# Kernel tuning notes

Hardware: AMD Instinct MI355X
Metric: run time of the kernel (lower is better)

Reference implementation:

```python
import jax, jax.numpy as jnp
import numpy as np

NUM_HEADS = 16


def setup_inputs() -> dict:
    key = jax.random.key(0)
    k1, k2, k3 = jax.random.split(key, 3)
    B, N, C = 2, 2048, 1024
    x = jax.random.normal(k1, (B, N, C), dtype=jnp.float32)
    w_qkv = jax.random.normal(k2, (3 * C, C), dtype=jnp.float32) * (C ** -0.5)
    w_proj = jax.random.normal(k3, (C, C), dtype=jnp.float32) * (C ** -0.5)
    b_proj = jnp.zeros((C,), dtype=jnp.float32)
    return {"x": x, "w_qkv": w_qkv, "w_proj": w_proj, "b_proj": b_proj}


def reference(x, w_qkv, w_proj, b_proj):
    B, N, C = x.shape
    H = NUM_HEADS
    D = C // H
    scale = 1.0 / jnp.sqrt(jnp.asarray(D, x.dtype))
    qkv = (x @ w_qkv.T).reshape(B, N, 3, H, D)
    qkv = jnp.transpose(qkv, (2, 0, 3, 1, 4))  # [3,B,H,N,D]
    q, k, v = qkv[0], qkv[1], qkv[2]
    # scaled dot-product attention with explicit score matrix [B,H,N,N]
    attn = jnp.einsum('bhnd,bhmd->bhnm', q, k) * scale
    attn = jax.nn.softmax(attn, axis=-1)
    out = jnp.einsum('bhnm,bhmd->bhnd', attn, v)
    out = jnp.transpose(out, (0, 2, 1, 3)).reshape(B, N, C)
    # output projection
    return out @ w_proj.T + b_proj
```

## Files before the change

### kernel.cpp

```cpp
#include <hip/hip_runtime.h>

typedef unsigned short u16;
typedef __attribute__((ext_vector_type(8))) short bf16x8;
typedef __attribute__((ext_vector_type(4))) float f32x4;

#define B_ 2
#define N_ 2048
#define C_ 1024
#define H_ 16
#define D_ 64
#define M_ (B_ * N_)

#define QSCALE 0.18033688011114336f

#define EXP2R(x) __builtin_amdgcn_exp2f(x)

__device__ __forceinline__ u16 f2bf(float f) {
    union { float f; unsigned u; } x; x.f = f;
    return (u16)((x.u + 0x8000u) >> 16);
}
__device__ __forceinline__ unsigned pack2bf(float a, float b) {
    union { float f; unsigned u; } x, y; x.f = a; y.f = b;
    return __builtin_amdgcn_perm(y.u + 0x8000u, x.u + 0x8000u, 0x07060302);
}

__device__ __forceinline__ void async_copy16(const void* gsrc, void* ldst) {
    __builtin_amdgcn_global_load_lds(
        (__attribute__((address_space(1))) void*)gsrc,
        (__attribute__((address_space(3))) void*)ldst,
        16, 0, 0);
}

__global__ void cast3_kernel(const float* __restrict__ x, const float* __restrict__ wq,
                             const float* __restrict__ wp, u16* __restrict__ xo,
                             u16* __restrict__ wqo, u16* __restrict__ wpo) {
    int b = blockIdx.x;
    const float* s; u16* d;
    if (b < 4096)      { s = x;  d = xo;  }
    else if (b < 7168) { s = wq; d = wqo; b -= 4096; }
    else               { s = wp; d = wpo; b -= 7168; }
    int i = (b * 256 + threadIdx.x) * 4;
    const float4 v = *(const float4*)(s + i);
    uint2 o;
    o.x = pack2bf(v.x, v.y);
    o.y = pack2bf(v.z, v.w);
    *(uint2*)(d + i) = o;
}

template <int EPI>
__global__ __launch_bounds__(256, 2) void gemm_bt(
    const u16* __restrict__ A, const u16* __restrict__ Bm,
    int M, int Ncols, int K, int ntiles_n,
    u16* __restrict__ qo, u16* __restrict__ ko, u16* __restrict__ vt,
    const float* __restrict__ bias, float* __restrict__ out) {
    __shared__ u16 As[128 * 64];
    __shared__ u16 Bs[128 * 64];
    const int tid = threadIdx.x, lane = tid & 63, w = tid >> 6;
    const int bx = blockIdx.x % ntiles_n, by = blockIdx.x / ntiles_n;
    const int m0 = by * 128, n0 = bx * 128;
    const int wm = w >> 1, wn = w & 1;
    const int q16 = lane >> 4, l15 = lane & 15;
    const int r0 = lane >> 3, c0 = (lane & 7) * 8;
    f32x4 acc[4][4] = {};

    for (int k0 = 0; k0 < K; k0 += 64) {
#pragma unroll
        for (int i = 0; i < 4; ++i) {
            int blk = w * 4 + i;
            int r = blk * 8 + r0;
            async_copy16(A + (size_t)(m0 + r) * K + k0 + c0, (char*)As + blk * 1024);
            async_copy16(Bm + (size_t)(n0 + r) * K + k0 + c0, (char*)Bs + blk * 1024);
        }
        __builtin_amdgcn_s_waitcnt(0);
        __syncthreads();
#pragma unroll
        for (int ks = 0; ks < 2; ++ks) {
            bf16x8 af[4], bf[4];
#pragma unroll
            for (int i = 0; i < 4; ++i) {
                af[i] = *(const bf16x8*)&As[(wm * 64 + i * 16 + l15) * 64 + ks * 32 + q16 * 8];
                bf[i] = *(const bf16x8*)&Bs[(wn * 64 + i * 16 + l15) * 64 + ks * 32 + q16 * 8];
            }
#pragma unroll
            for (int mi = 0; mi < 4; ++mi)
#pragma unroll
                for (int ni = 0; ni < 4; ++ni)
                    acc[mi][ni] = __builtin_amdgcn_mfma_f32_16x16x32_bf16(af[mi], bf[ni], acc[mi][ni], 0, 0, 0);
        }
        __syncthreads();
    }

#pragma unroll
    for (int mi = 0; mi < 4; ++mi) {
#pragma unroll
        for (int ni = 0; ni < 4; ++ni) {
            int n_g = n0 + wn * 64 + ni * 16 + l15;
            if (EPI == 0) {
                int which = n_g >> 10;
                int h = (n_g >> 6) & 15;
                int d = n_g & 63;
                int m_base = m0 + wm * 64 + mi * 16 + q16 * 4;
                int b = m_base >> 11;
                int nn0 = m_base & 2047;
                if (which == 2) {
                    uint2 pk;
                    pk.x = pack2bf(acc[mi][ni][0], acc[mi][ni][1]);
                    pk.y = pack2bf(acc[mi][ni][2], acc[mi][ni][3]);
                    *(uint2*)(vt + ((size_t)((b * H_ + h) * D_ + d) << 11) + nn0) = pk;
                } else {
                    size_t base = ((size_t)((b * H_ + h) * N_ + nn0) << 6) + d;
#pragma unroll
                    for (int r = 0; r < 4; ++r) {
                        float v = acc[mi][ni][r];
                        if (which == 0) qo[base + (size_t)r * D_] = f2bf(v * QSCALE);
                        else            ko[base + (size_t)r * D_] = f2bf(v);
                    }
                }
            } else {
#pragma unroll
                for (int r = 0; r < 4; ++r) {
                    int m_g = m0 + wm * 64 + mi * 16 + q16 * 4 + r;
                    out[(size_t)m_g * Ncols + n_g] = acc[mi][ni][r] + bias[n_g];
                }
            }
        }
    }
}

__global__ __launch_bounds__(256, 3) void attn_kernel(
    const u16* __restrict__ Q, const u16* __restrict__ K,
    const u16* __restrict__ VT, u16* __restrict__ O) {
    __shared__ u16 Ks[2][64 * 64];
    __shared__ u16 Vs[2][64 * 64];
    __shared__ u16 Ps[4][32 * 68];
    const int tid = threadIdx.x, lane = tid & 63, w = tid >> 6;
    const int q16 = lane >> 4, l15 = lane & 15;
    const int l7 = l15 & 7;
    const int bh = blockIdx.x >> 4;
    const int q0 = (blockIdx.x & 15) * 128;
    const size_t head = (size_t)bh * N_ * D_;
    const int lr3 = lane >> 3, lc7 = lane & 7;

    auto stage = [&](int kt, int buf) {
        int key0 = kt * 64;
#pragma unroll
        for (int i = 0; i < 2; ++i) {
            int c = w * 2 + i;
            int row = c * 8 + lr3;
            async_copy16(K + head + (size_t)(key0 + row) * D_ + (lc7 ^ lr3) * 8,
                         (char*)Ks[buf] + c * 1024);
            async_copy16(VT + head + (size_t)row * N_ + key0 + (lc7 ^ lr3) * 8,
                         (char*)Vs[buf] + c * 1024);
        }
    };

    stage(0, 0);
    bf16x8 qf[2][2];
#pragma unroll
    for (int f = 0; f < 2; ++f)
#pragma unroll
        for (int ks = 0; ks < 2; ++ks)
            qf[f][ks] = *(const bf16x8*)(Q + head + (size_t)(q0 + w * 32 + f * 16 + l15) * D_ +
                                         ks * 32 + q16 * 8);
    __builtin_amdgcn_s_waitcnt(0);
    __syncthreads();

    f32x4 o_acc[2][4] = {};
    float rs[2] = {0.f, 0.f};

    for (int kt = 0; kt < 32; ++kt) {
        int buf = kt & 1;
        if (kt + 1 < 32) stage(kt + 1, buf ^ 1);

#pragma unroll
        for (int kb = 0; kb < 4; ++kb) {
            f32x4 st[2] = {};
#pragma unroll
            for (int ks = 0; ks < 2; ++ks) {
                bf16x8 kf = *(const bf16x8*)&Ks[buf][(kb * 16 + l15) * 64 + ((ks * 4 + q16) ^ l7) * 8];
#pragma unroll
                for (int f = 0; f < 2; ++f)
                    st[f] = __builtin_amdgcn_mfma_f32_16x16x32_bf16(kf, qf[f][ks], st[f], 0, 0, 0);
            }
#pragma unroll
            for (int f = 0; f < 2; ++f) {
                float p0 = EXP2R(st[f][0]), p1 = EXP2R(st[f][1]);
                float p2 = EXP2R(st[f][2]), p3 = EXP2R(st[f][3]);
                rs[f] += (p0 + p1) + (p2 + p3);
                uint2 pk;
                pk.x = pack2bf(p0, p1);
                pk.y = pack2bf(p2, p3);
                *(uint2*)&Ps[w][(f * 16 + l15) * 68 + kb * 16 + q16 * 4] = pk;
            }
        }
#pragma unroll
        for (int ks2 = 0; ks2 < 2; ++ks2) {
            bf16x8 pf[2];
#pragma unroll
            for (int f = 0; f < 2; ++f)
                pf[f] = *(const bf16x8*)&Ps[w][(f * 16 + l15) * 68 + ks2 * 32 + q16 * 8];
#pragma unroll
            for (int di = 0; di < 4; ++di) {
                bf16x8 vf = *(const bf16x8*)&Vs[buf][(di * 16 + l15) * 64 + ((ks2 * 4 + q16) ^ l7) * 8];
#pragma unroll
                for (int f = 0; f < 2; ++f)
                    o_acc[f][di] = __builtin_amdgcn_mfma_f32_16x16x32_bf16(pf[f], vf, o_acc[f][di], 0, 0, 0);
            }
        }
        __builtin_amdgcn_s_waitcnt(0);
        __syncthreads();
    }

#pragma unroll
    for (int f = 0; f < 2; ++f) {
        rs[f] += __shfl_xor(rs[f], 16);
        rs[f] += __shfl_xor(rs[f], 32);
    }

    const int b = bh >> 4, h = bh & 15;
#pragma unroll
    for (int f = 0; f < 2; ++f) {
        float inv[4];
#pragma unroll
        for (int r = 0; r < 4; ++r) inv[r] = 1.0f / __shfl(rs[f], q16 * 4 + r);
#pragma unroll
        for (int di = 0; di < 4; ++di) {
            int d = di * 16 + l15;
#pragma unroll
            for (int r = 0; r < 4; ++r) {
                int qg = q0 + w * 32 + f * 16 + q16 * 4 + r;
                O[((size_t)(b * N_ + qg) << 10) + h * 64 + d] = f2bf(o_acc[f][di][r] * inv[r]);
            }
        }
    }
}

extern "C" void kernel_launch(void* const* d_in, const int* in_sizes, int n_in,
                              void* d_out, int out_size, void* d_ws, size_t ws_size,
                              hipStream_t stream) {
    const float* x      = (const float*)d_in[0];
    const float* w_qkv  = (const float*)d_in[1];
    const float* w_proj = (const float*)d_in[2];
    const float* b_proj = (const float*)d_in[3];
    float* out = (float*)d_out;

    char* ws = (char*)d_ws;
    const size_t MB = 1024 * 1024;
    u16* x_bf     = (u16*)(ws + 0 * MB);
    u16* wqkv_bf  = (u16*)(ws + 8 * MB);
    u16* wproj_bf = (u16*)(ws + 14 * MB);
    u16* q_bf     = (u16*)(ws + 16 * MB);
    u16* k_bf     = (u16*)(ws + 24 * MB);
    u16* vt_bf    = (u16*)(ws + 32 * MB);
    u16* ao_bf    = (u16*)(ws + 40 * MB);

    cast3_kernel<<<8192, 256, 0, stream>>>(x, w_qkv, w_proj, x_bf, wqkv_bf, wproj_bf);

    gemm_bt<0><<<32 * 24, 256, 0, stream>>>(x_bf, wqkv_bf, M_, 3 * C_, C_, 24,
                                            q_bf, k_bf, vt_bf, nullptr, nullptr);

    attn_kernel<<<512, 256, 0, stream>>>(q_bf, k_bf, vt_bf, ao_bf);

    gemm_bt<1><<<32 * 8, 256, 0, stream>>>(ao_bf, wproj_bf, M_, C_, C_, 8,
                                           nullptr, nullptr, nullptr, b_proj, out);
}
```

Baseline: 200.5 us.

## Split attention key range across two wave groups with LDS merge of partials

The attention block grows to 512 threads. Two groups of four waves each process half of the key sequence for the same 128 queries, and their unnormalized outputs and row sums are combined through shared memory at the end. The double-buffered async prefetch is replaced by single-buffer load-then-compute per group, which exposes load latency that more resident waves must hide. The GEMM launch bound is raised to 3 blocks per CU to push occupancy, which may cost registers.

```diff
diff --git a/kernel.cpp b/kernel.cpp
--- a/kernel.cpp
+++ b/kernel.cpp
@@ -48,7 +48,7 @@
 }
 
 template <int EPI>
-__global__ __launch_bounds__(256, 2) void gemm_bt(
+__global__ __launch_bounds__(256, 3) void gemm_bt(
     const u16* __restrict__ A, const u16* __restrict__ Bm,
     int M, int Ncols, int K, int ntiles_n,
     u16* __restrict__ qo, u16* __restrict__ ko, u16* __restrict__ vt,
@@ -127,57 +127,58 @@
     }
 }
 
-__global__ __launch_bounds__(256, 3) void attn_kernel(
+__global__ __launch_bounds__(512, 4) void attn_kernel(
     const u16* __restrict__ Q, const u16* __restrict__ K,
     const u16* __restrict__ VT, u16* __restrict__ O) {
-    __shared__ u16 Ks[2][64 * 64];
-    __shared__ u16 Vs[2][64 * 64];
-    __shared__ u16 Ps[4][32 * 68];
+    __shared__ __align__(16) char smem[67584];
+    u16* Ks = (u16*)smem;
+    u16* Vs = (u16*)(smem + 16384);
+    u16* Ps = (u16*)(smem + 32768);
+    float* Cn = (float*)smem;
+    float* Cl = (float*)(smem + 33792);
     const int tid = threadIdx.x, lane = tid & 63, w = tid >> 6;
+    const int g = w >> 2, wq = w & 3;
     const int q16 = lane >> 4, l15 = lane & 15;
     const int l7 = l15 & 7;
     const int bh = blockIdx.x >> 4;
     const int q0 = (blockIdx.x & 15) * 128;
     const size_t head = (size_t)bh * N_ * D_;
     const int lr3 = lane >> 3, lc7 = lane & 7;
-
-    auto stage = [&](int kt, int buf) {
-        int key0 = kt * 64;
+    u16* Ksg = Ks + g * 4096;
+    u16* Vsg = Vs + g * 4096;
+    u16* Psw = Ps + w * (32 * 68);
+
+    bf16x8 qf[2][2];
+#pragma unroll
+    for (int f = 0; f < 2; ++f)
+#pragma unroll
+        for (int ks = 0; ks < 2; ++ks)
+            qf[f][ks] = *(const bf16x8*)(Q + head + (size_t)(q0 + wq * 32 + f * 16 + l15) * D_ +
+                                         ks * 32 + q16 * 8);
+
+    f32x4 o_acc[2][4] = {};
+    float rs[2] = {0.f, 0.f};
+
+    for (int ktl = 0; ktl < 16; ++ktl) {
+        int key0 = g * 1024 + ktl * 64;
 #pragma unroll
         for (int i = 0; i < 2; ++i) {
-            int c = w * 2 + i;
+            int c = wq * 2 + i;
             int row = c * 8 + lr3;
             async_copy16(K + head + (size_t)(key0 + row) * D_ + (lc7 ^ lr3) * 8,
-                         (char*)Ks[buf] + c * 1024);
+                         (char*)Ksg + c * 1024);
             async_copy16(VT + head + (size_t)row * N_ + key0 + (lc7 ^ lr3) * 8,
-                         (char*)Vs[buf] + c * 1024);
-        }
-    };
-
-    stage(0, 0);
-    bf16x8 qf[2][2];
-#pragma unroll
-    for (int f = 0; f < 2; ++f)
-#pragma unroll
-        for (int ks = 0; ks < 2; ++ks)
-            qf[f][ks] = *(const bf16x8*)(Q + head + (size_t)(q0 + w * 32 + f * 16 + l15) * D_ +
-                                         ks * 32 + q16 * 8);
-    __builtin_amdgcn_s_waitcnt(0);
-    __syncthreads();
-
-    f32x4 o_acc[2][4] = {};
-    float rs[2] = {0.f, 0.f};
-
-    for (int kt = 0; kt < 32; ++kt) {
-        int buf = kt & 1;
-        if (kt + 1 < 32) stage(kt + 1, buf ^ 1);
+                         (char*)Vsg + c * 1024);
+        }
+        __builtin_amdgcn_s_waitcnt(0);
+        __syncthreads();
 
 #pragma unroll
         for (int kb = 0; kb < 4; ++kb) {
             f32x4 st[2] = {};
 #pragma unroll
             for (int ks = 0; ks < 2; ++ks) {
-                bf16x8 kf = *(const bf16x8*)&Ks[buf][(kb * 16 + l15) * 64 + ((ks * 4 + q16) ^ l7) * 8];
+                bf16x8 kf = *(const bf16x8*)&Ksg[(kb * 16 + l15) * 64 + ((ks * 4 + q16) ^ l7) * 8];
 #pragma unroll
                 for (int f = 0; f < 2; ++f)
                     st[f] = __builtin_amdgcn_mfma_f32_16x16x32_bf16(kf, qf[f][ks], st[f], 0, 0, 0);
@@ -190,7 +191,7 @@
                 uint2 pk;
                 pk.x = pack2bf(p0, p1);
                 pk.y = pack2bf(p2, p3);
-                *(uint2*)&Ps[w][(f * 16 + l15) * 68 + kb * 16 + q16 * 4] = pk;
+                *(uint2*)&Psw[(f * 16 + l15) * 68 + kb * 16 + q16 * 4] = pk;
             }
         }
 #pragma unroll
@@ -198,16 +199,15 @@
             bf16x8 pf[2];
 #pragma unroll
             for (int f = 0; f < 2; ++f)
-                pf[f] = *(const bf16x8*)&Ps[w][(f * 16 + l15) * 68 + ks2 * 32 + q16 * 8];
+                pf[f] = *(const bf16x8*)&Psw[(f * 16 + l15) * 68 + ks2 * 32 + q16 * 8];
 #pragma unroll
             for (int di = 0; di < 4; ++di) {
-                bf16x8 vf = *(const bf16x8*)&Vs[buf][(di * 16 + l15) * 64 + ((ks2 * 4 + q16) ^ l7) * 8];
+                bf16x8 vf = *(const bf16x8*)&Vsg[(di * 16 + l15) * 64 + ((ks2 * 4 + q16) ^ l7) * 8];
 #pragma unroll
                 for (int f = 0; f < 2; ++f)
                     o_acc[f][di] = __builtin_amdgcn_mfma_f32_16x16x32_bf16(pf[f], vf, o_acc[f][di], 0, 0, 0);
             }
         }
-        __builtin_amdgcn_s_waitcnt(0);
         __syncthreads();
     }
 
@@ -217,19 +217,39 @@
         rs[f] += __shfl_xor(rs[f], 32);
     }
 
-    const int b = bh >> 4, h = bh & 15;
-#pragma unroll
-    for (int f = 0; f < 2; ++f) {
-        float inv[4];
-#pragma unroll
-        for (int r = 0; r < 4; ++r) inv[r] = 1.0f / __shfl(rs[f], q16 * 4 + r);
-#pragma unroll
-        for (int di = 0; di < 4; ++di) {
-            int d = di * 16 + l15;
-#pragma unroll
-            for (int r = 0; r < 4; ++r) {
-                int qg = q0 + w * 32 + f * 16 + q16 * 4 + r;
-                O[((size_t)(b * N_ + qg) << 10) + h * 64 + d] = f2bf(o_acc[f][di][r] * inv[r]);
+    if (g == 1) {
+#pragma unroll
+        for (int f = 0; f < 2; ++f) {
+#pragma unroll
+            for (int di = 0; di < 4; ++di)
+#pragma unroll
+                for (int r = 0; r < 4; ++r)
+                    Cn[(wq * 32 + f * 16 + q16 * 4 + r) * 66 + di * 16 + l15] = o_acc[f][di][r];
+        }
+        if (q16 == 0) {
+            Cl[wq * 32 + l15] = rs[0];
+            Cl[wq * 32 + 16 + l15] = rs[1];
+        }
+    }
+    __syncthreads();
+    if (g == 0) {
+        const int b = bh >> 4, h = bh & 15;
+#pragma unroll
+        for (int f = 0; f < 2; ++f) {
+            float inv[4];
+#pragma unroll
+            for (int r = 0; r < 4; ++r)
+                inv[r] = 1.0f / (__shfl(rs[f], q16 * 4 + r) + Cl[wq * 32 + f * 16 + q16 * 4 + r]);
+#pragma unroll
+            for (int di = 0; di < 4; ++di) {
+                int d = di * 16 + l15;
+#pragma unroll
+                for (int r = 0; r < 4; ++r) {
+                    int qg = q0 + wq * 32 + f * 16 + q16 * 4 + r;
+                    float num = o_acc[f][di][r] +
+                                Cn[(wq * 32 + f * 16 + q16 * 4 + r) * 66 + d];
+                    O[((size_t)(b * N_ + qg) << 10) + h * 64 + d] = f2bf(num * inv[r]);
+                }
             }
         }
     }
@@ -259,7 +279,7 @@
     gemm_bt<0><<<32 * 24, 256, 0, stream>>>(x_bf, wqkv_bf, M_, 3 * C_, C_, 24,
                                             q_bf, k_bf, vt_bf, nullptr, nullptr);
 
-    attn_kernel<<<512, 256, 0, stream>>>(q_bf, k_bf, vt_bf, ao_bf);
+    attn_kernel<<<512, 512, 0, stream>>>(q_bf, k_bf, vt_bf, ao_bf);
 
     gemm_bt<1><<<32 * 8, 256, 0, stream>>>(ao_bf, wproj_bf, M_, C_, C_, 8,
                                            nullptr, nullptr, nullptr, b_proj, out);
```

Result: slower. 206.7 us (+3.1%).

## Halve attention query tile to 64 rows and double grid, swizzle P buffer

Applied to the files above, without the earlier changes.

The attention kernel now gives each wave 16 query rows instead of 32, so a block covers 64 queries and the grid doubles to 1024 blocks. The P scratch buffer uses an XOR swizzle in place of padding to avoid LDS bank conflicts, and launch bounds are raised for both the attention and GEMM kernels to allow more resident blocks per CU. This trades K/V reuse per block (each K/V tile is now loaded for half as many queries) for more parallelism and occupancy. The prefetch is also made unconditional by wrapping the tile index, which adds one redundant load on the last iteration.

```diff
diff --git a/kernel.cpp b/kernel.cpp
--- a/kernel.cpp
+++ b/kernel.cpp
@@ -48,7 +48,7 @@
 }
 
 template <int EPI>
-__global__ __launch_bounds__(256, 2) void gemm_bt(
+__global__ __launch_bounds__(256, 3) void gemm_bt(
     const u16* __restrict__ A, const u16* __restrict__ Bm,
     int M, int Ncols, int K, int ntiles_n,
     u16* __restrict__ qo, u16* __restrict__ ko, u16* __restrict__ vt,
@@ -127,17 +127,17 @@
     }
 }
 
-__global__ __launch_bounds__(256, 3) void attn_kernel(
+__global__ __launch_bounds__(256, 4) void attn_kernel(
     const u16* __restrict__ Q, const u16* __restrict__ K,
     const u16* __restrict__ VT, u16* __restrict__ O) {
     __shared__ u16 Ks[2][64 * 64];
     __shared__ u16 Vs[2][64 * 64];
-    __shared__ u16 Ps[4][32 * 68];
+    __shared__ u16 Ps[4][16 * 64];
     const int tid = threadIdx.x, lane = tid & 63, w = tid >> 6;
     const int q16 = lane >> 4, l15 = lane & 15;
     const int l7 = l15 & 7;
-    const int bh = blockIdx.x >> 4;
-    const int q0 = (blockIdx.x & 15) * 128;
+    const int bh = blockIdx.x >> 5;
+    const int q0 = (blockIdx.x & 31) * 64;
     const size_t head = (size_t)bh * N_ * D_;
     const int lr3 = lane >> 3, lc7 = lane & 7;
 
@@ -154,83 +154,68 @@
         }
     };
 
+    bf16x8 qf[2];
+#pragma unroll
+    for (int ks = 0; ks < 2; ++ks)
+        qf[ks] = *(const bf16x8*)(Q + head + (size_t)(q0 + w * 16 + l15) * D_ + ks * 32 + q16 * 8);
     stage(0, 0);
-    bf16x8 qf[2][2];
-#pragma unroll
-    for (int f = 0; f < 2; ++f)
-#pragma unroll
-        for (int ks = 0; ks < 2; ++ks)
-            qf[f][ks] = *(const bf16x8*)(Q + head + (size_t)(q0 + w * 32 + f * 16 + l15) * D_ +
-                                         ks * 32 + q16 * 8);
     __builtin_amdgcn_s_waitcnt(0);
     __syncthreads();
 
-    f32x4 o_acc[2][4] = {};
-    float rs[2] = {0.f, 0.f};
+    f32x4 o_acc[4] = {};
+    float rs = 0.f;
 
     for (int kt = 0; kt < 32; ++kt) {
         int buf = kt & 1;
-        if (kt + 1 < 32) stage(kt + 1, buf ^ 1);
+        stage((kt + 1) & 31, buf ^ 1);
 
 #pragma unroll
         for (int kb = 0; kb < 4; ++kb) {
-            f32x4 st[2] = {};
+            f32x4 st = {};
 #pragma unroll
             for (int ks = 0; ks < 2; ++ks) {
                 bf16x8 kf = *(const bf16x8*)&Ks[buf][(kb * 16 + l15) * 64 + ((ks * 4 + q16) ^ l7) * 8];
-#pragma unroll
-                for (int f = 0; f < 2; ++f)
-                    st[f] = __builtin_amdgcn_mfma_f32_16x16x32_bf16(kf, qf[f][ks], st[f], 0, 0, 0);
-            }
-#pragma unroll
-            for (int f = 0; f < 2; ++f) {
-                float p0 = EXP2R(st[f][0]), p1 = EXP2R(st[f][1]);
-                float p2 = EXP2R(st[f][2]), p3 = EXP2R(st[f][3]);
-                rs[f] += (p0 + p1) + (p2 + p3);
-                uint2 pk;
-                pk.x = pack2bf(p0, p1);
-                pk.y = pack2bf(p2, p3);
-                *(uint2*)&Ps[w][(f * 16 + l15) * 68 + kb * 16 + q16 * 4] = pk;
-            }
-        }
+                st = __builtin_amdgcn_mfma_f32_16x16x32_bf16(kf, qf[ks], st, 0, 0, 0);
+            }
+            float p0 = EXP2R(st[0]), p1 = EXP2R(st[1]);
+            float p2 = EXP2R(st[2]), p3 = EXP2R(st[3]);
+            rs += (p0 + p1) + (p2 + p3);
+            uint2 pk;
+            pk.x = pack2bf(p0, p1);
+            pk.y = pack2bf(p2, p3);
+            int bw = kb * 2 + (q16 >> 1), h = q16 & 1;
+            *(uint2*)&Ps[w][l15 * 64 + ((bw ^ l7) * 8 + h * 4)] = pk;
+        }
+
 #pragma unroll
         for (int ks2 = 0; ks2 < 2; ++ks2) {
-            bf16x8 pf[2];
-#pragma unroll
-            for (int f = 0; f < 2; ++f)
-                pf[f] = *(const bf16x8*)&Ps[w][(f * 16 + l15) * 68 + ks2 * 32 + q16 * 8];
+            int br = ks2 * 4 + q16;
+            bf16x8 pf = *(const bf16x8*)&Ps[w][l15 * 64 + (br ^ l7) * 8];
 #pragma unroll
             for (int di = 0; di < 4; ++di) {
                 bf16x8 vf = *(const bf16x8*)&Vs[buf][(di * 16 + l15) * 64 + ((ks2 * 4 + q16) ^ l7) * 8];
-#pragma unroll
-                for (int f = 0; f < 2; ++f)
-                    o_acc[f][di] = __builtin_amdgcn_mfma_f32_16x16x32_bf16(pf[f], vf, o_acc[f][di], 0, 0, 0);
-            }
-        }
+                o_acc[di] = __builtin_amdgcn_mfma_f32_16x16x32_bf16(pf, vf, o_acc[di], 0, 0, 0);
+            }
+        }
+
         __builtin_amdgcn_s_waitcnt(0);
         __syncthreads();
     }
 
-#pragma unroll
-    for (int f = 0; f < 2; ++f) {
-        rs[f] += __shfl_xor(rs[f], 16);
-        rs[f] += __shfl_xor(rs[f], 32);
-    }
+    rs += __shfl_xor(rs, 16);
+    rs += __shfl_xor(rs, 32);
+    float inv[4];
+#pragma unroll
+    for (int r = 0; r < 4; ++r) inv[r] = 1.0f / __shfl(rs, q16 * 4 + r);
 
     const int b = bh >> 4, h = bh & 15;
 #pragma unroll
-    for (int f = 0; f < 2; ++f) {
-        float inv[4];
-#pragma unroll
-        for (int r = 0; r < 4; ++r) inv[r] = 1.0f / __shfl(rs[f], q16 * 4 + r);
-#pragma unroll
-        for (int di = 0; di < 4; ++di) {
-            int d = di * 16 + l15;
-#pragma unroll
-            for (int r = 0; r < 4; ++r) {
-                int qg = q0 + w * 32 + f * 16 + q16 * 4 + r;
-                O[((size_t)(b * N_ + qg) << 10) + h * 64 + d] = f2bf(o_acc[f][di][r] * inv[r]);
-            }
+    for (int di = 0; di < 4; ++di) {
+        int d = di * 16 + l15;
+#pragma unroll
+        for (int r = 0; r < 4; ++r) {
+            int qg = q0 + w * 16 + q16 * 4 + r;
+            O[((size_t)(b * N_ + qg) << 10) + h * 64 + d] = f2bf(o_acc[di][r] * inv[r]);
         }
     }
 }
@@ -259,7 +244,7 @@
     gemm_bt<0><<<32 * 24, 256, 0, stream>>>(x_bf, wqkv_bf, M_, 3 * C_, C_, 24,
                                             q_bf, k_bf, vt_bf, nullptr, nullptr);
 
-    attn_kernel<<<512, 256, 0, stream>>>(q_bf, k_bf, vt_bf, ao_bf);
+    attn_kernel<<<1024, 256, 0, stream>>>(q_bf, k_bf, vt_bf, ao_bf);
 
     gemm_bt<1><<<32 * 8, 256, 0, stream>>>(ao_bf, wproj_bf, M_, C_, C_, 8,
                                            nullptr, nullptr, nullptr, b_proj, out);
```

Measured after the change: 194.5 us. -3.0%, faster.
